# Performance work log

Hardware: AMD Instinct MI355X
Metric: run time of the kernel (lower is better)

The kernel has to match this reference:

```python
import jax, jax.numpy as jnp
import numpy as np

N_NODES = 50000
N_EDGES = 640000
N_FEAT = 512
HIDDEN = 128
N_CLASSES = 64


def setup_inputs() -> dict:
    key = jax.random.key(0)
    k1, k2, k3, k4, k5, k6 = jax.random.split(key, 6)
    x = jax.random.normal(k1, (N_NODES, N_FEAT), dtype=jnp.float32)
    edge_index = jax.random.randint(k2, (2, N_EDGES), 0, N_NODES, dtype=jnp.int32)
    # GCNConv weights (glorot-ish scale) and biases
    W1 = jax.random.normal(k3, (N_FEAT, HIDDEN), dtype=jnp.float32) / np.sqrt(N_FEAT)
    b1 = jnp.zeros((HIDDEN,), dtype=jnp.float32)
    W2 = jax.random.normal(k4, (HIDDEN, N_CLASSES), dtype=jnp.float32) / np.sqrt(HIDDEN)
    b2 = jnp.zeros((N_CLASSES,), dtype=jnp.float32)
    return {"x": x, "edge_index": edge_index, "W1": W1, "b1": b1, "W2": W2, "b2": b2}


def reference(x, edge_index, W1, b1, W2, b2):
    N = x.shape[0]
    # Add self-loops (PyG GCNConv default)
    loop = jnp.arange(N, dtype=edge_index.dtype)
    src = jnp.concatenate([edge_index[0], loop])
    dst = jnp.concatenate([edge_index[1], loop])
    # Symmetric normalization: deg computed over targets incl. self-loops
    deg = jax.ops.segment_sum(jnp.ones(src.shape[0], dtype=x.dtype), dst, num_segments=N)
    dinv = jax.lax.rsqrt(deg)  # deg >= 1 thanks to self-loops
    norm = dinv[src] * dinv[dst]  # [E+N]

    def gcn_conv(h, W, b):
        h = h @ W                          # dense transform first (smaller msg dim)
        msg = h[src] * norm[:, None]       # gather + normalize
        return jax.ops.segment_sum(msg, dst, num_segments=N) + b  # scatter-add + bias

    h = jax.nn.relu(gcn_conv(x, W1, b1))
    # F.dropout with training=False is identity (eval mode)
    return gcn_conv(h, W2, b2)
```

## Files before the change

kernel.cpp:

```cpp
#include <hip/hip_runtime.h>


#define NNODES 50000
#define NEDGES 640000
#define NFEAT 512
#define NHID 128
#define NCLS 64

__global__ void k_zero2(int* __restrict__ a, int* __restrict__ b, int n) {
  int i = blockIdx.x * blockDim.x + threadIdx.x;
  if (i < n) { a[i] = 0; b[i] = 0; }
}

__global__ void k_hist(const int* __restrict__ dst, int* __restrict__ indeg, int E) {
  int i = blockIdx.x * blockDim.x + threadIdx.x;
  if (i < E) atomicAdd(&indeg[dst[i]], 1);
}

__global__ void k_dinv(const int* __restrict__ indeg, float* __restrict__ dinv, int n) {
  int i = blockIdx.x * blockDim.x + threadIdx.x;
  if (i < n) dinv[i] = 1.0f / sqrtf((float)(indeg[i] + 1));
}

__global__ void k_scan_block(const int* __restrict__ indeg, int* __restrict__ row_start,
                             int* __restrict__ blocksum, int n) {
  __shared__ int sdata[256];
  int t = threadIdx.x;
  int base = blockIdx.x * 1024 + t * 4;
  int v[4];
#pragma unroll
  for (int j = 0; j < 4; ++j) v[j] = (base + j < n) ? indeg[base + j] : 0;
  int tsum = v[0] + v[1] + v[2] + v[3];
  sdata[t] = tsum;
  __syncthreads();
  for (int off = 1; off < 256; off <<= 1) {
    int x = (t >= off) ? sdata[t - off] : 0;
    __syncthreads();
    sdata[t] += x;
    __syncthreads();
  }
  int excl = sdata[t] - tsum;
  if (t == 255) blocksum[blockIdx.x] = sdata[255];
  int run = excl;
#pragma unroll
  for (int j = 0; j < 4; ++j) {
    if (base + j < n) { row_start[base + j] = run; run += v[j]; }
  }
}

__global__ void k_scan_top(const int* __restrict__ blocksum, int* __restrict__ blockoff, int nb) {
  if (threadIdx.x == 0 && blockIdx.x == 0) {
    int run = 0;
    for (int i = 0; i < nb; ++i) { blockoff[i] = run; run += blocksum[i]; }
  }
}

__global__ void k_scan_add(int* __restrict__ row_start, const int* __restrict__ blockoff,
                           int n, int E) {
  int i = blockIdx.x * blockDim.x + threadIdx.x;
  if (i < n) row_start[i] += blockoff[i >> 10];
  if (i == 0) row_start[n] = E;
}

__global__ void k_scatter(const int* __restrict__ src, const int* __restrict__ dst,
                          const int* __restrict__ row_start, int* __restrict__ cursor,
                          const float* __restrict__ dinv, int* __restrict__ csr_src,
                          float* __restrict__ csr_norm, int E) {
  int e = blockIdx.x * blockDim.x + threadIdx.x;
  if (e < E) {
    int s = src[e], d = dst[e];
    int pos = atomicAdd(&cursor[d], 1);
    int idx = row_start[d] + pos;
    csr_src[idx] = s;
    csr_norm[idx] = dinv[s] * dinv[d];
  }
}

template <int BM, int BN, int BK>
__global__ __launch_bounds__(128) void k_gemm(const float* __restrict__ A,
                                              const float* __restrict__ B,
                                              float* __restrict__ C, int M, int K) {
  constexpr int TXN = BN / 8;
  constexpr int TYN = 128 / TXN;
  static_assert(BM == TYN * 8, "tile mismatch");
  constexpr int S = BM + 4;
  __shared__ float As[BK][S];
  __shared__ float Bs[BK][BN];
  const int tid = threadIdx.x;
  const int tx = tid % TXN;
  const int ty = tid / TXN;
  const int row0 = blockIdx.x * BM;

  float acc[8][8];
#pragma unroll
  for (int i = 0; i < 8; ++i)
#pragma unroll
    for (int j = 0; j < 8; ++j) acc[i][j] = 0.f;

  for (int k0 = 0; k0 < K; k0 += BK) {
    constexpr int KQ = BK / 4;
    constexpr int AF4 = BM * BK / 4;
#pragma unroll
    for (int it = 0; it < AF4 / 128; ++it) {
      int v = tid + it * 128;
      int m = v / KQ;
      int kq = v % KQ;
      float4 val = make_float4(0.f, 0.f, 0.f, 0.f);
      if (row0 + m < M)
        val = *(const float4*)(A + (size_t)(row0 + m) * K + k0 + kq * 4);
      As[kq * 4 + 0][m] = val.x;
      As[kq * 4 + 1][m] = val.y;
      As[kq * 4 + 2][m] = val.z;
      As[kq * 4 + 3][m] = val.w;
    }
    constexpr int BF4 = BK * BN / 4;
    const float4* Bsrc = (const float4*)(B + (size_t)k0 * BN);
    float4* Bdst = (float4*)&Bs[0][0];
#pragma unroll
    for (int it = 0; it < BF4 / 128; ++it)
      Bdst[tid + it * 128] = Bsrc[tid + it * 128];
    __syncthreads();

#pragma unroll
    for (int kk = 0; kk < BK; ++kk) {
      float4 a0 = *(const float4*)&As[kk][ty * 4];
      float4 a1 = *(const float4*)&As[kk][BM / 2 + ty * 4];
      float4 b0 = *(const float4*)&Bs[kk][tx * 4];
      float4 b1 = *(const float4*)&Bs[kk][BN / 2 + tx * 4];
      float av[8] = {a0.x, a0.y, a0.z, a0.w, a1.x, a1.y, a1.z, a1.w};
      float bv[8] = {b0.x, b0.y, b0.z, b0.w, b1.x, b1.y, b1.z, b1.w};
#pragma unroll
      for (int i = 0; i < 8; ++i)
#pragma unroll
        for (int j = 0; j < 8; ++j) acc[i][j] += av[i] * bv[j];
    }
    __syncthreads();
  }

#pragma unroll
  for (int i = 0; i < 8; ++i) {
    int r = row0 + (i < 4 ? ty * 4 + i : BM / 2 + ty * 4 + (i - 4));
    if (r < M) {
      float4 o0 = {acc[i][0], acc[i][1], acc[i][2], acc[i][3]};
      float4 o1 = {acc[i][4], acc[i][5], acc[i][6], acc[i][7]};
      *(float4*)(C + (size_t)r * BN + tx * 4) = o0;
      *(float4*)(C + (size_t)r * BN + BN / 2 + tx * 4) = o1;
    }
  }
}

template <int F, bool RELU>
__global__ __launch_bounds__(F) void k_agg(const float* __restrict__ h,
                                           const float* __restrict__ bias,
                                           const int* __restrict__ row_start,
                                           const int* __restrict__ csr_src,
                                           const float* __restrict__ csr_norm,
                                           const float* __restrict__ dinv,
                                           float* __restrict__ out) {
  int n = blockIdx.x;
  int f = threadIdx.x;
  float dn = dinv[n];
  float acc0 = dn * dn * h[(size_t)n * F + f] + bias[f];
  float acc1 = 0.f, acc2 = 0.f, acc3 = 0.f;
  int e0 = row_start[n], e1 = row_start[n + 1];
  int e = e0;
  for (; e + 4 <= e1; e += 4) {
    int s0 = csr_src[e + 0]; float w0 = csr_norm[e + 0];
    int s1 = csr_src[e + 1]; float w1 = csr_norm[e + 1];
    int s2 = csr_src[e + 2]; float w2 = csr_norm[e + 2];
    int s3 = csr_src[e + 3]; float w3 = csr_norm[e + 3];
    acc0 += w0 * h[(size_t)s0 * F + f];
    acc1 += w1 * h[(size_t)s1 * F + f];
    acc2 += w2 * h[(size_t)s2 * F + f];
    acc3 += w3 * h[(size_t)s3 * F + f];
  }
  for (; e < e1; ++e) {
    int s = csr_src[e];
    acc0 += csr_norm[e] * h[(size_t)s * F + f];
  }
  float acc = (acc0 + acc1) + (acc2 + acc3);
  if (RELU) acc = fmaxf(acc, 0.f);
  out[(size_t)n * F + f] = acc;
}

static inline size_t align256(size_t x) { return (x + 255) & ~(size_t)255; }

extern "C" void kernel_launch(void* const* d_in, const int* in_sizes, int n_in,
                              void* d_out, int out_size, void* d_ws, size_t ws_size,
                              hipStream_t stream) {
  const float* x = (const float*)d_in[0];
  const int* edge = (const int*)d_in[1];
  const float* W1 = (const float*)d_in[2];
  const float* b1 = (const float*)d_in[3];
  const float* W2 = (const float*)d_in[4];
  const float* b2 = (const float*)d_in[5];
  float* out = (float*)d_out;

  const int N = NNODES;
  const int E = NEDGES;
  const int* src = edge;
  const int* dst = edge + E;

  char* w = (char*)d_ws;
  int* indeg = (int*)w;        w += align256((size_t)N * 4);
  int* cursor = (int*)w;       w += align256((size_t)N * 4);
  float* dinv = (float*)w;     w += align256((size_t)N * 4);
  int* row_start = (int*)w;    w += align256((size_t)(N + 1) * 4);
  int* blocksum = (int*)w;     w += align256(64 * 4);
  int* blockoff = (int*)w;     w += align256(64 * 4);
  int* csr_src = (int*)w;      w += align256((size_t)E * 4);
  float* csr_norm = (float*)w; w += align256((size_t)E * 4);
  float* h0 = (float*)w;       w += align256((size_t)N * NHID * 4);
  float* h1 = (float*)w;       w += align256((size_t)N * NHID * 4);
  float* h2 = (float*)w;       w += align256((size_t)N * NCLS * 4);

  const int nblk_n = (N + 255) / 256;
  const int nblk_e = (E + 255) / 256;
  const int nblk_scan = (N + 1023) / 1024;

  k_zero2<<<nblk_n, 256, 0, stream>>>(indeg, cursor, N);
  k_hist<<<nblk_e, 256, 0, stream>>>(dst, indeg, E);
  k_dinv<<<nblk_n, 256, 0, stream>>>(indeg, dinv, N);
  k_scan_block<<<nblk_scan, 256, 0, stream>>>(indeg, row_start, blocksum, N);
  k_scan_top<<<1, 64, 0, stream>>>(blocksum, blockoff, nblk_scan);
  k_scan_add<<<nblk_n, 256, 0, stream>>>(row_start, blockoff, N, E);
  k_scatter<<<nblk_e, 256, 0, stream>>>(src, dst, row_start, cursor, dinv,
                                        csr_src, csr_norm, E);

  k_gemm<64, NHID, 32><<<(N + 63) / 64, 128, 0, stream>>>(x, W1, h0, N, NFEAT);
  k_agg<NHID, true><<<N, NHID, 0, stream>>>(h0, b1, row_start, csr_src, csr_norm,
                                            dinv, h1);
  k_gemm<128, NCLS, 32><<<(N + 127) / 128, 128, 0, stream>>>(h1, W2, h2, N, NHID);
  k_agg<NCLS, false><<<N, NCLS, 0, stream>>>(h2, b2, row_start, csr_src, csr_norm,
                                             dinv, out);
}
```

Baseline: 428.1 us.

## Use split-fp16 MFMA GEMMs and emit hi/lo fp16 from first aggregation

Replaces the scalar FP32 tiled GEMMs with MFMA 16x16x32 f16 kernels that emulate FP32 precision by splitting operands into scaled hi/lo fp16 parts and doing three MFMA passes. Weights are pre-transposed and split by a small conversion kernel, and the first aggregation writes its output directly as hi/lo fp16 for the second GEMM. This aims to cut the dense transform cost by using matrix cores. In exchange it adds extra conversion work, LDS-free global operand loads, and an uncoalesced column-wise output store, with slightly reduced precision.

Result: faster. 410.9 us (-4.0%).

```diff
diff --git a/kernel.cpp b/kernel.cpp
--- a/kernel.cpp
+++ b/kernel.cpp
@@ -6,6 +6,9 @@
 #define NFEAT 512
 #define NHID 128
 #define NCLS 64
+
+typedef _Float16 f16x8 __attribute__((ext_vector_type(8)));
+typedef float f32x4 __attribute__((ext_vector_type(4)));
 
 __global__ void k_zero2(int* __restrict__ a, int* __restrict__ b, int n) {
   int i = blockIdx.x * blockDim.x + threadIdx.x;
@@ -76,87 +79,101 @@
   }
 }
 
-template <int BM, int BN, int BK>
-__global__ __launch_bounds__(128) void k_gemm(const float* __restrict__ A,
-                                              const float* __restrict__ B,
-                                              float* __restrict__ C, int M, int K) {
-  constexpr int TXN = BN / 8;
-  constexpr int TYN = 128 / TXN;
-  static_assert(BM == TYN * 8, "tile mismatch");
-  constexpr int S = BM + 4;
-  __shared__ float As[BK][S];
-  __shared__ float Bs[BK][BN];
-  const int tid = threadIdx.x;
-  const int tx = tid % TXN;
-  const int ty = tid / TXN;
-  const int row0 = blockIdx.x * BM;
-
-  float acc[8][8];
-#pragma unroll
-  for (int i = 0; i < 8; ++i)
-#pragma unroll
-    for (int j = 0; j < 8; ++j) acc[i][j] = 0.f;
-
-  for (int k0 = 0; k0 < K; k0 += BK) {
-    constexpr int KQ = BK / 4;
-    constexpr int AF4 = BM * BK / 4;
-#pragma unroll
-    for (int it = 0; it < AF4 / 128; ++it) {
-      int v = tid + it * 128;
-      int m = v / KQ;
-      int kq = v % KQ;
-      float4 val = make_float4(0.f, 0.f, 0.f, 0.f);
-      if (row0 + m < M)
-        val = *(const float4*)(A + (size_t)(row0 + m) * K + k0 + kq * 4);
-      As[kq * 4 + 0][m] = val.x;
-      As[kq * 4 + 1][m] = val.y;
-      As[kq * 4 + 2][m] = val.z;
-      As[kq * 4 + 3][m] = val.w;
+__global__ void k_wcvt(const float* __restrict__ W, _Float16* __restrict__ Wt_hi,
+                       _Float16* __restrict__ Wt_lo, int K, int Nc) {
+  int i = blockIdx.x * blockDim.x + threadIdx.x;
+  if (i < K * Nc) {
+    int k = i / Nc, n = i % Nc;
+    float v = W[i];
+    _Float16 h = (_Float16)v;
+    Wt_hi[(size_t)n * K + k] = h;
+    Wt_lo[(size_t)n * K + k] = (_Float16)((v - (float)h) * 1024.0f);
+  }
+}
+
+template <int K, int WY, int WX, bool AFP32>
+__global__ __launch_bounds__(256) void k_mfma_gemm(
+    const float* __restrict__ A32, const _Float16* __restrict__ Ahi,
+    const _Float16* __restrict__ Alo, const _Float16* __restrict__ Bhi,
+    const _Float16* __restrict__ Blo, float* __restrict__ C, int M, int N) {
+  const int wid = threadIdx.x >> 6;
+  const int lane = threadIdx.x & 63;
+  const int wy = wid / WX, wx = wid % WX;
+  const int r0 = (blockIdx.x * WY + wy) * 64;
+  const int c0 = (blockIdx.y * WX + wx) * 64;
+  const int lrow = lane & 15;
+  const int koff = (lane >> 4) * 8;
+
+  f32x4 acc_h[4][4] = {};
+  f32x4 acc_l[4][4] = {};
+
+  for (int k0 = 0; k0 < K; k0 += 32) {
+    f16x8 bh[4], bl[4];
+#pragma unroll
+    for (int cf = 0; cf < 4; ++cf) {
+      size_t boff = (size_t)(c0 + cf * 16 + lrow) * K + k0 + koff;
+      bh[cf] = *(const f16x8*)(Bhi + boff);
+      bl[cf] = *(const f16x8*)(Blo + boff);
     }
-    constexpr int BF4 = BK * BN / 4;
-    const float4* Bsrc = (const float4*)(B + (size_t)k0 * BN);
-    float4* Bdst = (float4*)&Bs[0][0];
-#pragma unroll
-    for (int it = 0; it < BF4 / 128; ++it)
-      Bdst[tid + it * 128] = Bsrc[tid + it * 128];
-    __syncthreads();
-
-#pragma unroll
-    for (int kk = 0; kk < BK; ++kk) {
-      float4 a0 = *(const float4*)&As[kk][ty * 4];
-      float4 a1 = *(const float4*)&As[kk][BM / 2 + ty * 4];
-      float4 b0 = *(const float4*)&Bs[kk][tx * 4];
-      float4 b1 = *(const float4*)&Bs[kk][BN / 2 + tx * 4];
-      float av[8] = {a0.x, a0.y, a0.z, a0.w, a1.x, a1.y, a1.z, a1.w};
-      float bv[8] = {b0.x, b0.y, b0.z, b0.w, b1.x, b1.y, b1.z, b1.w};
-#pragma unroll
-      for (int i = 0; i < 8; ++i)
-#pragma unroll
-        for (int j = 0; j < 8; ++j) acc[i][j] += av[i] * bv[j];
+#pragma unroll
+    for (int rf = 0; rf < 4; ++rf) {
+      int row = r0 + rf * 16 + lrow;
+      row = row < M ? row : M - 1;
+      f16x8 ah, al;
+      if (AFP32) {
+        const float* ap = A32 + (size_t)row * K + k0 + koff;
+        float4 v0 = *(const float4*)ap;
+        float4 v1 = *(const float4*)(ap + 4);
+        float vv[8] = {v0.x, v0.y, v0.z, v0.w, v1.x, v1.y, v1.z, v1.w};
+#pragma unroll
+        for (int j = 0; j < 8; ++j) {
+          _Float16 h = (_Float16)vv[j];
+          ah[j] = h;
+          al[j] = (_Float16)((vv[j] - (float)h) * 1024.0f);
+        }
+      } else {
+        size_t aoff = (size_t)row * K + k0 + koff;
+        ah = *(const f16x8*)(Ahi + aoff);
+        al = *(const f16x8*)(Alo + aoff);
+      }
+#pragma unroll
+      for (int cf = 0; cf < 4; ++cf) {
+        acc_h[rf][cf] =
+            __builtin_amdgcn_mfma_f32_16x16x32_f16(ah, bh[cf], acc_h[rf][cf], 0, 0, 0);
+        acc_l[rf][cf] =
+            __builtin_amdgcn_mfma_f32_16x16x32_f16(ah, bl[cf], acc_l[rf][cf], 0, 0, 0);
+        acc_l[rf][cf] =
+            __builtin_amdgcn_mfma_f32_16x16x32_f16(al, bh[cf], acc_l[rf][cf], 0, 0, 0);
+      }
     }
-    __syncthreads();
-  }
-
-#pragma unroll
-  for (int i = 0; i < 8; ++i) {
-    int r = row0 + (i < 4 ? ty * 4 + i : BM / 2 + ty * 4 + (i - 4));
-    if (r < M) {
-      float4 o0 = {acc[i][0], acc[i][1], acc[i][2], acc[i][3]};
-      float4 o1 = {acc[i][4], acc[i][5], acc[i][6], acc[i][7]};
-      *(float4*)(C + (size_t)r * BN + tx * 4) = o0;
-      *(float4*)(C + (size_t)r * BN + BN / 2 + tx * 4) = o1;
+  }
+
+#pragma unroll
+  for (int rf = 0; rf < 4; ++rf) {
+    if (r0 + rf * 16 >= M) continue;
+    int rbase = r0 + rf * 16 + (lane >> 4) * 4;
+#pragma unroll
+    for (int cf = 0; cf < 4; ++cf) {
+      int col = c0 + cf * 16 + lrow;
+#pragma unroll
+      for (int q = 0; q < 4; ++q) {
+        C[(size_t)(rbase + q) * N + col] =
+            acc_h[rf][cf][q] + acc_l[rf][cf][q] * (1.0f / 1024.0f);
+      }
     }
   }
 }
 
-template <int F, bool RELU>
+template <int F, bool RELU, bool EMIT16>
 __global__ __launch_bounds__(F) void k_agg(const float* __restrict__ h,
                                            const float* __restrict__ bias,
                                            const int* __restrict__ row_start,
                                            const int* __restrict__ csr_src,
                                            const float* __restrict__ csr_norm,
                                            const float* __restrict__ dinv,
-                                           float* __restrict__ out) {
+                                           float* __restrict__ out,
+                                           _Float16* __restrict__ out_hi,
+                                           _Float16* __restrict__ out_lo) {
   int n = blockIdx.x;
   int f = threadIdx.x;
   float dn = dinv[n];
@@ -180,7 +197,13 @@
   }
   float acc = (acc0 + acc1) + (acc2 + acc3);
   if (RELU) acc = fmaxf(acc, 0.f);
-  out[(size_t)n * F + f] = acc;
+  if (EMIT16) {
+    _Float16 hh = (_Float16)acc;
+    out_hi[(size_t)n * F + f] = hh;
+    out_lo[(size_t)n * F + f] = (_Float16)((acc - (float)hh) * 1024.0f);
+  } else {
+    out[(size_t)n * F + f] = acc;
+  }
 }
 
 static inline size_t align256(size_t x) { return (x + 255) & ~(size_t)255; }
@@ -202,17 +225,22 @@
   const int* dst = edge + E;
 
   char* w = (char*)d_ws;
-  int* indeg = (int*)w;        w += align256((size_t)N * 4);
-  int* cursor = (int*)w;       w += align256((size_t)N * 4);
-  float* dinv = (float*)w;     w += align256((size_t)N * 4);
-  int* row_start = (int*)w;    w += align256((size_t)(N + 1) * 4);
-  int* blocksum = (int*)w;     w += align256(64 * 4);
-  int* blockoff = (int*)w;     w += align256(64 * 4);
-  int* csr_src = (int*)w;      w += align256((size_t)E * 4);
-  float* csr_norm = (float*)w; w += align256((size_t)E * 4);
-  float* h0 = (float*)w;       w += align256((size_t)N * NHID * 4);
-  float* h1 = (float*)w;       w += align256((size_t)N * NHID * 4);
-  float* h2 = (float*)w;       w += align256((size_t)N * NCLS * 4);
+  int* indeg = (int*)w;          w += align256((size_t)N * 4);
+  int* cursor = (int*)w;         w += align256((size_t)N * 4);
+  float* dinv = (float*)w;       w += align256((size_t)N * 4);
+  int* row_start = (int*)w;      w += align256((size_t)(N + 1) * 4);
+  int* blocksum = (int*)w;       w += align256(64 * 4);
+  int* blockoff = (int*)w;       w += align256(64 * 4);
+  int* csr_src = (int*)w;        w += align256((size_t)E * 4);
+  float* csr_norm = (float*)w;   w += align256((size_t)E * 4);
+  _Float16* W1t_hi = (_Float16*)w; w += align256((size_t)NFEAT * NHID * 2);
+  _Float16* W1t_lo = (_Float16*)w; w += align256((size_t)NFEAT * NHID * 2);
+  _Float16* W2t_hi = (_Float16*)w; w += align256((size_t)NHID * NCLS * 2);
+  _Float16* W2t_lo = (_Float16*)w; w += align256((size_t)NHID * NCLS * 2);
+  float* h0 = (float*)w;         w += align256((size_t)N * NHID * 4);
+  _Float16* h1_hi = (_Float16*)w; w += align256((size_t)N * NHID * 2);
+  _Float16* h1_lo = (_Float16*)w; w += align256((size_t)N * NHID * 2);
+  float* h2 = (float*)w;         w += align256((size_t)N * NCLS * 4);
 
   const int nblk_n = (N + 255) / 256;
   const int nblk_e = (E + 255) / 256;
@@ -227,10 +255,25 @@
   k_scatter<<<nblk_e, 256, 0, stream>>>(src, dst, row_start, cursor, dinv,
                                         csr_src, csr_norm, E);
 
-  k_gemm<64, NHID, 32><<<(N + 63) / 64, 128, 0, stream>>>(x, W1, h0, N, NFEAT);
-  k_agg<NHID, true><<<N, NHID, 0, stream>>>(h0, b1, row_start, csr_src, csr_norm,
-                                            dinv, h1);
-  k_gemm<128, NCLS, 32><<<(N + 127) / 128, 128, 0, stream>>>(h1, W2, h2, N, NHID);
-  k_agg<NCLS, false><<<N, NCLS, 0, stream>>>(h2, b2, row_start, csr_src, csr_norm,
-                                             dinv, out);
-}
+  k_wcvt<<<(NFEAT * NHID + 255) / 256, 256, 0, stream>>>(W1, W1t_hi, W1t_lo,
+                                                         NFEAT, NHID);
+  k_wcvt<<<(NHID * NCLS + 255) / 256, 256, 0, stream>>>(W2, W2t_hi, W2t_lo,
+                                                        NHID, NCLS);
+
+  {
+    dim3 grid((N + 127) / 128, 1);
+    k_mfma_gemm<NFEAT, 2, 2, true><<<grid, 256, 0, stream>>>(
+        x, nullptr, nullptr, W1t_hi, W1t_lo, h0, N, NHID);
+  }
+  k_agg<NHID, true, true><<<N, NHID, 0, stream>>>(h0, b1, row_start, csr_src,
+                                                  csr_norm, dinv, nullptr,
+                                                  h1_hi, h1_lo);
+  {
+    dim3 grid((N + 255) / 256, 1);
+    k_mfma_gemm<NHID, 4, 1, false><<<grid, 256, 0, stream>>>(
+        nullptr, h1_hi, h1_lo, W2t_hi, W2t_lo, h2, N, NCLS);
+  }
+  k_agg<NCLS, false, false><<<N, NCLS, 0, stream>>>(h2, b2, row_start, csr_src,
+                                                    csr_norm, dinv, out,
+                                                    nullptr, nullptr);
+}
```
